# Optimization experiments

Measured on AMD Instinct MI355X. Metric: run time of the kernel, lower is better.

The kernel has to match this reference:

```python
import jax, jax.numpy as jnp
import numpy as np

ALPHA = 3.0
EPS = 1e-30


def setup_inputs() -> dict:
    key = jax.random.key(0)
    ks = jax.random.split(key, 12)
    B, N, T, D = 16, 2048, 96, 32
    s = 1.0 / np.sqrt(D)
    inp = {
        "spatial_nodes": jax.random.normal(ks[0], (B, N, D), dtype=jnp.float32),
        "temporal_nodes": jax.random.normal(ks[1], (B, T, D), dtype=jnp.float32),
        # ss graph linears (no bias)
        "W_ss1": jax.random.normal(ks[2], (D, D), dtype=jnp.float32) * s,
        "W_ss2": jax.random.normal(ks[3], (D, D), dtype=jnp.float32) * s,
        # 'st' attention (query/key linears with bias); value linear is unused in forward
        "Wq_st": jax.random.normal(ks[4], (D, D), dtype=jnp.float32) * s,
        "bq_st": jax.random.normal(ks[5], (D,), dtype=jnp.float32) * s,
        "Wk_st": jax.random.normal(ks[6], (D, D), dtype=jnp.float32) * s,
        "bk_st": jax.random.normal(ks[7], (D,), dtype=jnp.float32) * s,
        # 'ts' attention
        "Wq_ts": jax.random.normal(ks[8], (D, D), dtype=jnp.float32) * s,
        "bq_ts": jax.random.normal(ks[9], (D,), dtype=jnp.float32) * s,
        "Wk_ts": jax.random.normal(ks[10], (D, D), dtype=jnp.float32) * s,
        "bk_ts": jax.random.normal(ks[11], (D,), dtype=jnp.float32) * s,
    }
    return inp


def _uni_adj(a):
    # relu -> global-max normalize -> tanh -> nan_to_num (matches GraphConstructor.uni_adj)
    r = jax.nn.relu(a)
    div = jnp.max(r)  # global max across the whole tensor (incl. batch), as in torch
    out = jnp.tanh(jnp.where(div > 0, r / (div + EPS), r))
    return jnp.nan_to_num(out)


def reference(spatial_nodes, temporal_nodes, W_ss1, W_ss2,
              Wq_st, bq_st, Wk_st, bk_st, Wq_ts, bq_ts, Wk_ts, bk_ts):
    # forward() detaches both inputs
    s = jax.lax.stop_gradient(spatial_nodes)  # (B, N, D)
    t = jax.lax.stop_gradient(temporal_nodes)  # (B, T, D)
    N = s.shape[1]

    emb = jnp.concatenate([s, t], axis=1)  # (B, N+T, D)
    adj = jnp.einsum('bnf,bmf->bnm', emb, emb)  # (B, N+T, N+T)

    def ss_graph(x1, x2):
        n1 = jnp.tanh(ALPHA * (x1 @ W_ss1.T))
        n2 = jnp.tanh(ALPHA * (x2 @ W_ss2.T))
        return ALPHA * (jnp.einsum('bnf,bmf->bnm', n1, n2)
                        - jnp.einsum('bnf,bmf->bnm', n2, n1))

    def attn_graph(x1, x2, Wq, bq, Wk, bk):
        q = x1 @ Wq.T + bq
        k = x2 @ Wk.T + bk
        return jnp.einsum('bnf,bmf->bnm', q, k)

    ss_adj = adj[:, :N, :N] + ss_graph(s, s)
    st_adj = adj[:, :N, N:] + attn_graph(s, t, Wq_st, bq_st, Wk_st, bk_st)
    ts_adj = adj[:, N:, :N] + attn_graph(t, s, Wq_ts, bq_ts, Wk_ts, bk_ts)
    tt_adj = adj[:, N:, N:]

    ss_u = _uni_adj(ss_adj)
    st_u = _uni_adj(st_adj)
    ts_u = _uni_adj(ts_adj)
    tt_u = jnp.triu(_uni_adj(tt_adj))  # tt_mask=True: upper-triangular (incl diag)

    top = jnp.concatenate([ss_u, st_u], axis=2)
    bot = jnp.concatenate([ts_u, tt_u], axis=2)
    return jnp.concatenate([top, bot], axis=1)  # (B, N+T, N+T)
```

## Files before the change

### kernel.cpp

```cpp
#include <hip/hip_runtime.h>
#include <math.h>

#define BATCH 16
#define NS 2048
#define NT 96
#define DIM 32
#define ROWL 2144
#define EPSV 1e-30f

#define FS_STRIDE 224
#define FT_STRIDE 96

typedef __attribute__((ext_vector_type(8))) short bf16x8;
typedef __attribute__((ext_vector_type(4))) float f32x4;

__device__ __forceinline__ ushort f2bf_rn(float x){
  uint u = __float_as_uint(x);
  return (ushort)((u + 0x7FFFu + ((u >> 16) & 1u)) >> 16);
}
__device__ __forceinline__ float bf2f(ushort h){
  return __uint_as_float(((uint)h) << 16);
}

__global__ __launch_bounds__(256) void feat_kernel(
    const float* __restrict__ sp, const float* __restrict__ tp,
    const float* __restrict__ Wss1, const float* __restrict__ Wss2,
    const float* __restrict__ Wqst, const float* __restrict__ bqst,
    const float* __restrict__ Wkst, const float* __restrict__ bkst,
    const float* __restrict__ Wqts, const float* __restrict__ bqts,
    const float* __restrict__ Wkts, const float* __restrict__ bkts,
    ushort* __restrict__ FShi, ushort* __restrict__ FSlo,
    ushort* __restrict__ FThi, ushort* __restrict__ FTlo)
{
  __shared__ float Wl[6*1056];
  __shared__ float bl[128];
  __shared__ float xl[8][32];
  const int tid = threadIdx.x;
  {
    const float* Ws[6] = {Wss1, Wss2, Wqst, Wkst, Wqts, Wkts};
    #pragma unroll
    for (int m = 0; m < 6; m++){
      const float* W = Ws[m];
      #pragma unroll
      for (int c = 0; c < 4; c++){
        int idx = c*256 + tid;
        Wl[m*1056 + (idx>>5)*33 + (idx&31)] = W[idx];
      }
    }
    if (tid < 32)        bl[tid] = bqst[tid];
    else if (tid < 64)   bl[tid] = bkst[tid-32];
    else if (tid < 96)   bl[tid] = bqts[tid-64];
    else if (tid < 128)  bl[tid] = bkts[tid-96];
  }
  const int rs = tid >> 5;
  const int f  = tid & 31;
  const int row = blockIdx.x*8 + rs;
  const int NROWS = BATCH*NS;
  const int TOT   = NROWS + BATCH*NT;
  const bool valid = row < TOT;
  const bool isS   = row < NROWS;
  if (valid){
    const float* xp = isS ? (sp + (size_t)row*DIM) : (tp + (size_t)(row-NROWS)*DIM);
    xl[rs][f] = xp[f];
  }
  __syncthreads();
  if (!valid) return;

  if (isS){
    float a1=0.f, a2=0.f, aq=0.f, ak=0.f;
    #pragma unroll
    for (int d=0; d<32; d++){
      float xv = xl[rs][d];
      a1 = fmaf(xv, Wl[0*1056 + f*33 + d], a1);
      a2 = fmaf(xv, Wl[1*1056 + f*33 + d], a2);
      aq = fmaf(xv, Wl[2*1056 + f*33 + d], aq);
      ak = fmaf(xv, Wl[5*1056 + f*33 + d], ak);
    }
    float n1 = tanhf(3.0f*a1);
    float n2 = tanhf(3.0f*a2);
    float vals[7];
    vals[0] = xl[rs][f];
    vals[1] = 3.0f*n1;
    vals[2] = -3.0f*n2;
    vals[3] = n2;
    vals[4] = n1;
    vals[5] = aq + bl[0  + f];
    vals[6] = ak + bl[96 + f];
    ushort* oh = FShi + (size_t)row*FS_STRIDE + f;
    ushort* ol = FSlo + (size_t)row*FS_STRIDE + f;
    #pragma unroll
    for (int sgm = 0; sgm < 7; sgm++){
      float x = vals[sgm];
      ushort h = f2bf_rn(x);
      oh[sgm*32] = h;
      ol[sgm*32] = f2bf_rn(x - bf2f(h));
    }
  } else {
    const int rt = row - NROWS;
    float aq=0.f, ak=0.f;
    #pragma unroll
    for (int d=0; d<32; d++){
      float xv = xl[rs][d];
      aq = fmaf(xv, Wl[4*1056 + f*33 + d], aq);
      ak = fmaf(xv, Wl[3*1056 + f*33 + d], ak);
    }
    float vals[3];
    vals[0] = xl[rs][f];
    vals[1] = aq + bl[64 + f];
    vals[2] = ak + bl[32 + f];
    ushort* oh = FThi + (size_t)rt*FT_STRIDE + f;
    ushort* ol = FTlo + (size_t)rt*FT_STRIDE + f;
    #pragma unroll
    for (int sgm = 0; sgm < 3; sgm++){
      float x = vals[sgm];
      ushort h = f2bf_rn(x);
      oh[sgm*32] = h;
      ol[sgm*32] = f2bf_rn(x - bf2f(h));
    }
  }
}

template<int K>
__device__ __forceinline__ void stage64(const ushort* __restrict__ src, int stride,
    int nrows, int row0, int o0, int o1, int o2, ushort* __restrict__ dst)
{
  constexpr int CPR = K/8;
  constexpr int KP  = K + 8;
  for (int u = threadIdx.x; u < 64*CPR; u += 256){
    int row  = u / CPR;
    int cell = u - row*CPR;
    int seg  = cell >> 2;
    int ko   = (cell & 3)*8;
    int so   = (seg == 0) ? o0 : ((seg == 1) ? o1 : o2);
    uint4 v = make_uint4(0u,0u,0u,0u);
    int g = row0 + row;
    if (g < nrows) v = *(const uint4*)(src + (size_t)g*stride + so + ko);
    *(uint4*)(dst + row*KP + cell*8) = v;
  }
}

template<int K>
__global__ __launch_bounds__(256) void adj_mfma(
    const ushort* __restrict__ Uhi, const ushort* __restrict__ Ulo, int ustride,
    int NI, int uo0, int uo1, int uo2,
    const ushort* __restrict__ Vhi, const ushort* __restrict__ Vlo, int vstride,
    int NJ, int vo0, int vo1, int vo2,
    float* __restrict__ out, int i0g, int j0g, float* __restrict__ maxslot)
{
  constexpr int KP = K + 8;
  __shared__ __align__(16) ushort sUhi[64*KP];
  __shared__ __align__(16) ushort sUlo[64*KP];
  __shared__ __align__(16) ushort sVhi[64*KP];
  __shared__ __align__(16) ushort sVlo[64*KP];
  __shared__ float red[4];
  const int tid = threadIdx.x;
  const int b   = blockIdx.z;
  const int i0t = blockIdx.y*64;
  const int j0t = blockIdx.x*64;

  stage64<K>(Uhi + (size_t)b*NI*ustride, ustride, NI, i0t, uo0,uo1,uo2, sUhi);
  stage64<K>(Ulo + (size_t)b*NI*ustride, ustride, NI, i0t, uo0,uo1,uo2, sUlo);
  stage64<K>(Vhi + (size_t)b*NJ*vstride, vstride, NJ, j0t, vo0,vo1,vo2, sVhi);
  stage64<K>(Vlo + (size_t)b*NJ*vstride, vstride, NJ, j0t, vo0,vo1,vo2, sVlo);
  __syncthreads();

  const int lane = tid & 63;
  const int w    = tid >> 6;
  const int wm   = w >> 1;
  const int wn   = w & 1;
  const int l15  = lane & 15;
  const int l4   = lane >> 4;

  f32x4 acc[2][2] = {};

  #pragma unroll
  for (int kb = 0; kb < K/32; ++kb){
    const int kof = kb*32 + l4*8;
    bf16x8 ah0 = *(const bf16x8*)&sUhi[(wm*32 +  0 + l15)*KP + kof];
    bf16x8 ah1 = *(const bf16x8*)&sUhi[(wm*32 + 16 + l15)*KP + kof];
    bf16x8 al0 = *(const bf16x8*)&sUlo[(wm*32 +  0 + l15)*KP + kof];
    bf16x8 al1 = *(const bf16x8*)&sUlo[(wm*32 + 16 + l15)*KP + kof];
    bf16x8 bh0 = *(const bf16x8*)&sVhi[(wn*32 +  0 + l15)*KP + kof];
    bf16x8 bh1 = *(const bf16x8*)&sVhi[(wn*32 + 16 + l15)*KP + kof];
    bf16x8 bl0 = *(const bf16x8*)&sVlo[(wn*32 +  0 + l15)*KP + kof];
    bf16x8 bl1 = *(const bf16x8*)&sVlo[(wn*32 + 16 + l15)*KP + kof];

    acc[0][0] = __builtin_amdgcn_mfma_f32_16x16x32_bf16(ah0, bh0, acc[0][0], 0,0,0);
    acc[0][0] = __builtin_amdgcn_mfma_f32_16x16x32_bf16(ah0, bl0, acc[0][0], 0,0,0);
    acc[0][0] = __builtin_amdgcn_mfma_f32_16x16x32_bf16(al0, bh0, acc[0][0], 0,0,0);

    acc[0][1] = __builtin_amdgcn_mfma_f32_16x16x32_bf16(ah0, bh1, acc[0][1], 0,0,0);
    acc[0][1] = __builtin_amdgcn_mfma_f32_16x16x32_bf16(ah0, bl1, acc[0][1], 0,0,0);
    acc[0][1] = __builtin_amdgcn_mfma_f32_16x16x32_bf16(al0, bh1, acc[0][1], 0,0,0);

    acc[1][0] = __builtin_amdgcn_mfma_f32_16x16x32_bf16(ah1, bh0, acc[1][0], 0,0,0);
    acc[1][0] = __builtin_amdgcn_mfma_f32_16x16x32_bf16(ah1, bl0, acc[1][0], 0,0,0);
    acc[1][0] = __builtin_amdgcn_mfma_f32_16x16x32_bf16(al1, bh0, acc[1][0], 0,0,0);

    acc[1][1] = __builtin_amdgcn_mfma_f32_16x16x32_bf16(ah1, bh1, acc[1][1], 0,0,0);
    acc[1][1] = __builtin_amdgcn_mfma_f32_16x16x32_bf16(ah1, bl1, acc[1][1], 0,0,0);
    acc[1][1] = __builtin_amdgcn_mfma_f32_16x16x32_bf16(al1, bh1, acc[1][1], 0,0,0);
  }

  float lmax = 0.f;
  const size_t obase = (size_t)b*ROWL*ROWL;
  #pragma unroll
  for (int sm = 0; sm < 2; sm++){
    #pragma unroll
    for (int sn = 0; sn < 2; sn++){
      #pragma unroll
      for (int r = 0; r < 4; r++){
        int gi = i0t + wm*32 + sm*16 + l4*4 + r;
        int gj = j0t + wn*32 + sn*16 + l15;
        if (gi < NI && gj < NJ){
          float v = acc[sm][sn][r];
          out[obase + (size_t)(i0g+gi)*ROWL + (j0g+gj)] = v;
          lmax = fmaxf(lmax, v);
        }
      }
    }
  }
  #pragma unroll
  for (int off = 32; off > 0; off >>= 1)
    lmax = fmaxf(lmax, __shfl_xor(lmax, off));
  if ((tid & 63) == 0) red[tid >> 6] = lmax;
  __syncthreads();
  if (tid == 0){
    float m4 = fmaxf(fmaxf(red[0], red[1]), fmaxf(red[2], red[3]));
    atomicMax((int*)maxslot, __float_as_int(m4));
  }
}

__device__ __forceinline__ float tanh01(float x){
  float e = __expf(2.0f*x);
  return __fdividef(e - 1.0f, e + 1.0f);
}
__device__ __forceinline__ float4 uni4(float4 v, float r){
  v.x = tanh01(fmaxf(v.x,0.f)*r);
  v.y = tanh01(fmaxf(v.y,0.f)*r);
  v.z = tanh01(fmaxf(v.z,0.f)*r);
  v.w = tanh01(fmaxf(v.w,0.f)*r);
  return v;
}

__global__ __launch_bounds__(256) void uni_kernel(float* __restrict__ out,
                                                  const float* __restrict__ mx)
{
  const int row = blockIdx.x;
  const int i   = row % ROWL;
  const bool top = (i < NS);
  const float rl = 1.0f/((top ? mx[0] : mx[2]) + EPSV);
  const float rr = 1.0f/((top ? mx[1] : mx[3]) + EPSV);
  float4* rowp = (float4*)(out + (size_t)row*ROWL);
  const int tid = threadIdx.x;

  rowp[tid]       = uni4(rowp[tid],       rl);
  rowp[tid + 256] = uni4(rowp[tid + 256], rl);

  if (tid < 24){
    float4 v = uni4(rowp[tid + 512], rr);
    if (!top){
      int il = i - NS;
      int jl = 4*tid;
      if (jl+0 < il) v.x = 0.f;
      if (jl+1 < il) v.y = 0.f;
      if (jl+2 < il) v.z = 0.f;
      if (jl+3 < il) v.w = 0.f;
    }
    rowp[tid + 512] = v;
  }
}

extern "C" void kernel_launch(void* const* d_in, const int* in_sizes, int n_in,
                              void* d_out, int out_size, void* d_ws, size_t ws_size,
                              hipStream_t stream)
{
  const float* sp   = (const float*)d_in[0];
  const float* tp   = (const float*)d_in[1];
  const float* Wss1 = (const float*)d_in[2];
  const float* Wss2 = (const float*)d_in[3];
  const float* Wqst = (const float*)d_in[4];
  const float* bqst = (const float*)d_in[5];
  const float* Wkst = (const float*)d_in[6];
  const float* bkst = (const float*)d_in[7];
  const float* Wqts = (const float*)d_in[8];
  const float* bqts = (const float*)d_in[9];
  const float* Wkts = (const float*)d_in[10];
  const float* bkts = (const float*)d_in[11];
  float* out  = (float*)d_out;
  float* wsf  = (float*)d_ws;
  float* maxs = wsf;

  const size_t SHROWS = (size_t)BATCH*NS;
  const size_t STROWS = (size_t)BATCH*NT;
  ushort* FShi = (ushort*)(wsf + 16);
  ushort* FSlo = FShi + SHROWS*FS_STRIDE;
  ushort* FThi = FSlo + SHROWS*FS_STRIDE;
  ushort* FTlo = FThi + STROWS*FT_STRIDE;

  feat_kernel<<<dim3((BATCH*(NS+NT))/8), 256, 0, stream>>>(
      sp,tp,Wss1,Wss2,Wqst,bqst,Wkst,bkst,Wqts,bqts,Wkts,bkts,
      FShi,FSlo,FThi,FTlo);

  adj_mfma<96><<<dim3(32,32,BATCH), 256, 0, stream>>>(
      FShi,FSlo,FS_STRIDE,NS, 0,32,64,
      FShi,FSlo,FS_STRIDE,NS, 0,96,128,
      out, 0,0, maxs+0);

  adj_mfma<64><<<dim3(2,32,BATCH), 256, 0, stream>>>(
      FShi,FSlo,FS_STRIDE,NS, 0,160,0,
      FThi,FTlo,FT_STRIDE,NT, 0,64,0,
      out, 0,NS, maxs+1);

  adj_mfma<64><<<dim3(32,2,BATCH), 256, 0, stream>>>(
      FThi,FTlo,FT_STRIDE,NT, 0,32,0,
      FShi,FSlo,FS_STRIDE,NS, 0,192,0,
      out, NS,0, maxs+2);

  adj_mfma<32><<<dim3(2,2,BATCH), 256, 0, stream>>>(
      FThi,FTlo,FT_STRIDE,NT, 0,0,0,
      FThi,FTlo,FT_STRIDE,NT, 0,0,0,
      out, NS,NS, maxs+3);

  uni_kernel<<<BATCH*ROWL, 256, 0, stream>>>(out, maxs);
}
```

Before: 638.8 us.

## Widen adj MFMA tiles to 64x128 with fragment-ordered LDS layout

The adjacency MFMA kernel now computes 64x128 output tiles (2x4 MFMA tiles per wave) instead of 64x64, halving the number of blocks along j and reusing each A fragment across four B fragments. Shared memory is laid out in MFMA-fragment order, so each lane reads one contiguous 16-byte cell per operand, replacing padded row-major tiles. Launch bounds request two blocks per CU. This raises per-thread accumulator register use and LDS per block, and the write epilogue loops rows outer, columns inner.

After: 548.7 us. 14.1% less time.

```diff
diff --git a/kernel.cpp b/kernel.cpp
--- a/kernel.cpp
+++ b/kernel.cpp
@@ -120,102 +120,124 @@
   }
 }
 
-template<int K>
-__device__ __forceinline__ void stage64(const ushort* __restrict__ src, int stride,
-    int nrows, int row0, int o0, int o1, int o2, ushort* __restrict__ dst)
-{
-  constexpr int CPR = K/8;
-  constexpr int KP  = K + 8;
-  for (int u = threadIdx.x; u < 64*CPR; u += 256){
-    int row  = u / CPR;
-    int cell = u - row*CPR;
-    int seg  = cell >> 2;
-    int ko   = (cell & 3)*8;
-    int so   = (seg == 0) ? o0 : ((seg == 1) ? o1 : o2);
-    uint4 v = make_uint4(0u,0u,0u,0u);
-    int g = row0 + row;
-    if (g < nrows) v = *(const uint4*)(src + (size_t)g*stride + so + ko);
-    *(uint4*)(dst + row*KP + cell*8) = v;
-  }
-}
-
-template<int K>
-__global__ __launch_bounds__(256) void adj_mfma(
+template<int NKB>
+__global__ __launch_bounds__(256, 2) void adj_mfma(
     const ushort* __restrict__ Uhi, const ushort* __restrict__ Ulo, int ustride,
     int NI, int uo0, int uo1, int uo2,
     const ushort* __restrict__ Vhi, const ushort* __restrict__ Vlo, int vstride,
     int NJ, int vo0, int vo1, int vo2,
     float* __restrict__ out, int i0g, int j0g, float* __restrict__ maxslot)
 {
-  constexpr int KP = K + 8;
-  __shared__ __align__(16) ushort sUhi[64*KP];
-  __shared__ __align__(16) ushort sUlo[64*KP];
-  __shared__ __align__(16) ushort sVhi[64*KP];
-  __shared__ __align__(16) ushort sVlo[64*KP];
+  constexpr int ACELLS = 4*NKB*64;
+  constexpr int BCELLS = 8*NKB*64;
+  __shared__ __align__(16) ushort sAh[ACELLS*8];
+  __shared__ __align__(16) ushort sAl[ACELLS*8];
+  __shared__ __align__(16) ushort sBh[BCELLS*8];
+  __shared__ __align__(16) ushort sBl[BCELLS*8];
   __shared__ float red[4];
   const int tid = threadIdx.x;
   const int b   = blockIdx.z;
   const int i0t = blockIdx.y*64;
-  const int j0t = blockIdx.x*64;
-
-  stage64<K>(Uhi + (size_t)b*NI*ustride, ustride, NI, i0t, uo0,uo1,uo2, sUhi);
-  stage64<K>(Ulo + (size_t)b*NI*ustride, ustride, NI, i0t, uo0,uo1,uo2, sUlo);
-  stage64<K>(Vhi + (size_t)b*NJ*vstride, vstride, NJ, j0t, vo0,vo1,vo2, sVhi);
-  stage64<K>(Vlo + (size_t)b*NJ*vstride, vstride, NJ, j0t, vo0,vo1,vo2, sVlo);
+  const int j0t = blockIdx.x*128;
+
+  const ushort* Ubh = Uhi + (size_t)b*NI*ustride;
+  const ushort* Ubl = Ulo + (size_t)b*NI*ustride;
+  const ushort* Vbh = Vhi + (size_t)b*NJ*vstride;
+  const ushort* Vbl = Vlo + (size_t)b*NJ*vstride;
+
+  for (int u = tid; u < ACELLS; u += 256){
+    int q   = u & 3;
+    int t   = u >> 2;
+    int r15 = t & 15;
+    int t2  = t >> 4;
+    int kb  = t2 % NKB;
+    int g   = t2 / NKB;
+    int so  = (kb == 0) ? uo0 : ((kb == 1) ? uo1 : uo2);
+    int gr  = i0t + g*16 + r15;
+    uint4 vh = make_uint4(0u,0u,0u,0u), vl = vh;
+    if (gr < NI){
+      const size_t base = (size_t)gr*ustride + so + q*8;
+      vh = *(const uint4*)(Ubh + base);
+      vl = *(const uint4*)(Ubl + base);
+    }
+    int dcell = (t2*4 + q)*16 + r15;
+    *(uint4*)&sAh[dcell*8] = vh;
+    *(uint4*)&sAl[dcell*8] = vl;
+  }
+  for (int u = tid; u < BCELLS; u += 256){
+    int q   = u & 3;
+    int t   = u >> 2;
+    int r15 = t & 15;
+    int t2  = t >> 4;
+    int kb  = t2 % NKB;
+    int g   = t2 / NKB;
+    int so  = (kb == 0) ? vo0 : ((kb == 1) ? vo1 : vo2);
+    int gr  = j0t + g*16 + r15;
+    uint4 vh = make_uint4(0u,0u,0u,0u), vl = vh;
+    if (gr < NJ){
+      const size_t base = (size_t)gr*vstride + so + q*8;
+      vh = *(const uint4*)(Vbh + base);
+      vl = *(const uint4*)(Vbl + base);
+    }
+    int dcell = (t2*4 + q)*16 + r15;
+    *(uint4*)&sBh[dcell*8] = vh;
+    *(uint4*)&sBl[dcell*8] = vl;
+  }
   __syncthreads();
 
   const int lane = tid & 63;
   const int w    = tid >> 6;
-  const int wm   = w >> 1;
-  const int wn   = w & 1;
+  const int wm   = w & 1;
+  const int wn   = w >> 1;
   const int l15  = lane & 15;
   const int l4   = lane >> 4;
 
-  f32x4 acc[2][2] = {};
+  f32x4 acc[2][4] = {};
 
   #pragma unroll
-  for (int kb = 0; kb < K/32; ++kb){
-    const int kof = kb*32 + l4*8;
-    bf16x8 ah0 = *(const bf16x8*)&sUhi[(wm*32 +  0 + l15)*KP + kof];
-    bf16x8 ah1 = *(const bf16x8*)&sUhi[(wm*32 + 16 + l15)*KP + kof];
-    bf16x8 al0 = *(const bf16x8*)&sUlo[(wm*32 +  0 + l15)*KP + kof];
-    bf16x8 al1 = *(const bf16x8*)&sUlo[(wm*32 + 16 + l15)*KP + kof];
-    bf16x8 bh0 = *(const bf16x8*)&sVhi[(wn*32 +  0 + l15)*KP + kof];
-    bf16x8 bh1 = *(const bf16x8*)&sVhi[(wn*32 + 16 + l15)*KP + kof];
-    bf16x8 bl0 = *(const bf16x8*)&sVlo[(wn*32 +  0 + l15)*KP + kof];
-    bf16x8 bl1 = *(const bf16x8*)&sVlo[(wn*32 + 16 + l15)*KP + kof];
-
-    acc[0][0] = __builtin_amdgcn_mfma_f32_16x16x32_bf16(ah0, bh0, acc[0][0], 0,0,0);
-    acc[0][0] = __builtin_amdgcn_mfma_f32_16x16x32_bf16(ah0, bl0, acc[0][0], 0,0,0);
-    acc[0][0] = __builtin_amdgcn_mfma_f32_16x16x32_bf16(al0, bh0, acc[0][0], 0,0,0);
-
-    acc[0][1] = __builtin_amdgcn_mfma_f32_16x16x32_bf16(ah0, bh1, acc[0][1], 0,0,0);
-    acc[0][1] = __builtin_amdgcn_mfma_f32_16x16x32_bf16(ah0, bl1, acc[0][1], 0,0,0);
-    acc[0][1] = __builtin_amdgcn_mfma_f32_16x16x32_bf16(al0, bh1, acc[0][1], 0,0,0);
-
-    acc[1][0] = __builtin_amdgcn_mfma_f32_16x16x32_bf16(ah1, bh0, acc[1][0], 0,0,0);
-    acc[1][0] = __builtin_amdgcn_mfma_f32_16x16x32_bf16(ah1, bl0, acc[1][0], 0,0,0);
-    acc[1][0] = __builtin_amdgcn_mfma_f32_16x16x32_bf16(al1, bh0, acc[1][0], 0,0,0);
-
-    acc[1][1] = __builtin_amdgcn_mfma_f32_16x16x32_bf16(ah1, bh1, acc[1][1], 0,0,0);
-    acc[1][1] = __builtin_amdgcn_mfma_f32_16x16x32_bf16(ah1, bl1, acc[1][1], 0,0,0);
-    acc[1][1] = __builtin_amdgcn_mfma_f32_16x16x32_bf16(al1, bh1, acc[1][1], 0,0,0);
+  for (int kb = 0; kb < NKB; ++kb){
+    bf16x8 ah[2], al[2], bh[4], bl[4];
+    #pragma unroll
+    for (int m = 0; m < 2; m++){
+      int off = ((2*wm + m)*NKB + kb)*512 + lane*8;
+      ah[m] = *(const bf16x8*)&sAh[off];
+      al[m] = *(const bf16x8*)&sAl[off];
+    }
+    #pragma unroll
+    for (int n = 0; n < 4; n++){
+      int off = ((4*wn + n)*NKB + kb)*512 + lane*8;
+      bh[n] = *(const bf16x8*)&sBh[off];
+      bl[n] = *(const bf16x8*)&sBl[off];
+    }
+    #pragma unroll
+    for (int m = 0; m < 2; m++){
+      #pragma unroll
+      for (int n = 0; n < 4; n++){
+        acc[m][n] = __builtin_amdgcn_mfma_f32_16x16x32_bf16(ah[m], bh[n], acc[m][n], 0,0,0);
+        acc[m][n] = __builtin_amdgcn_mfma_f32_16x16x32_bf16(ah[m], bl[n], acc[m][n], 0,0,0);
+        acc[m][n] = __builtin_amdgcn_mfma_f32_16x16x32_bf16(al[m], bh[n], acc[m][n], 0,0,0);
+      }
+    }
   }
 
   float lmax = 0.f;
   const size_t obase = (size_t)b*ROWL*ROWL;
   #pragma unroll
-  for (int sm = 0; sm < 2; sm++){
-    #pragma unroll
-    for (int sn = 0; sn < 2; sn++){
-      #pragma unroll
-      for (int r = 0; r < 4; r++){
-        int gi = i0t + wm*32 + sm*16 + l4*4 + r;
-        int gj = j0t + wn*32 + sn*16 + l15;
-        if (gi < NI && gj < NJ){
-          float v = acc[sm][sn][r];
-          out[obase + (size_t)(i0g+gi)*ROWL + (j0g+gj)] = v;
-          lmax = fmaxf(lmax, v);
+  for (int m = 0; m < 2; m++){
+    int gi_base = i0t + wm*32 + m*16 + l4*4;
+    #pragma unroll
+    for (int r = 0; r < 4; r++){
+      int gi = gi_base + r;
+      if (gi < NI){
+        const size_t rowb = obase + (size_t)(i0g+gi)*ROWL + j0g;
+        #pragma unroll
+        for (int n = 0; n < 4; n++){
+          int gj = j0t + wn*64 + n*16 + l15;
+          if (gj < NJ){
+            float v = acc[m][n][r];
+            out[rowb + gj] = v;
+            lmax = fmaxf(lmax, v);
+          }
         }
       }
     }
@@ -302,22 +324,22 @@
       sp,tp,Wss1,Wss2,Wqst,bqst,Wkst,bkst,Wqts,bqts,Wkts,bkts,
       FShi,FSlo,FThi,FTlo);
 
-  adj_mfma<96><<<dim3(32,32,BATCH), 256, 0, stream>>>(
+  adj_mfma<3><<<dim3(16,32,BATCH), 256, 0, stream>>>(
       FShi,FSlo,FS_STRIDE,NS, 0,32,64,
       FShi,FSlo,FS_STRIDE,NS, 0,96,128,
       out, 0,0, maxs+0);
 
-  adj_mfma<64><<<dim3(2,32,BATCH), 256, 0, stream>>>(
+  adj_mfma<2><<<dim3(1,32,BATCH), 256, 0, stream>>>(
       FShi,FSlo,FS_STRIDE,NS, 0,160,0,
       FThi,FTlo,FT_STRIDE,NT, 0,64,0,
       out, 0,NS, maxs+1);
 
-  adj_mfma<64><<<dim3(32,2,BATCH), 256, 0, stream>>>(
+  adj_mfma<2><<<dim3(16,2,BATCH), 256, 0, stream>>>(
       FThi,FTlo,FT_STRIDE,NT, 0,32,0,
       FShi,FSlo,FS_STRIDE,NS, 0,192,0,
       out, NS,0, maxs+2);
 
-  adj_mfma<32><<<dim3(2,2,BATCH), 256, 0, stream>>>(
+  adj_mfma<1><<<dim3(1,2,BATCH), 256, 0, stream>>>(
       FThi,FTlo,FT_STRIDE,NT, 0,0,0,
       FThi,FTlo,FT_STRIDE,NT, 0,0,0,
       out, NS,NS, maxs+3);
```
